# Kernel tuning notes

Measured on AMD Instinct MI355X. Metric: run time of the kernel, lower is better.

## Reference

```python
import jax, jax.numpy as jnp
import numpy as np

N = 100000      # nodes
E = 3200000     # edges (avg degree 32)
D = 128         # embed_dim
STEP = 1        # number of gnn_conv steps


def setup_inputs() -> dict:
    key = jax.random.key(0)
    k1, k2, k3, k4, k5 = jax.random.split(key, 5)
    hidden = jax.random.normal(k1, (N, D), dtype=jnp.float32)
    src = jax.random.randint(k2, (E,), 0, N)
    dst = jax.random.randint(k3, (E,), 0, N)
    # nn.Linear(D, 3D, bias=False) -> store transposed as [D, 3D] for h @ W
    W_h = jax.random.normal(k4, (D, 3 * D), dtype=jnp.float32) * 0.05
    W_hf = jax.random.normal(k5, (D, 2 * D), dtype=jnp.float32) * 0.05
    return {"hidden": hidden, "src": src, "dst": dst, "W_h": W_h, "W_hf": W_hf}


def _graph_conv(h, src, dst, n):
    # DGL GraphConv(norm='both', weight=False, bias=False):
    # h_dst = d_in(dst)^{-1/2} * sum_{(src->dst)} d_out(src)^{-1/2} * h_src
    ones = jnp.ones(src.shape[0], dtype=h.dtype)
    out_deg = jnp.clip(jax.ops.segment_sum(ones, src, num_segments=n), 1.0)
    in_deg = jnp.clip(jax.ops.segment_sum(ones, dst, num_segments=n), 1.0)
    h_norm = h * jax.lax.rsqrt(out_deg)[:, None]          # [N, D]
    agg = jax.ops.segment_sum(h_norm[src], dst, num_segments=n)  # [N, D]
    return agg * jax.lax.rsqrt(in_deg)[:, None]


def reference(hidden, src, dst, W_h, W_hf):
    n = hidden.shape[0]
    seqs = []
    for _ in range(STEP):
        h1, h2, h3 = jnp.split(hidden @ W_h, 3, axis=-1)   # each [N, D]
        conv = _graph_conv(h1, src, dst, n)                 # sparse aggregation
        f1, f2 = jnp.split(conv @ W_hf, 2, axis=-1)         # each [N, D]
        gate = jax.nn.relu(f1 + h2)
        hidden = h3 + gate * f2
        seqs.append(hidden)
    return hidden, jnp.stack(seqs, axis=1).mean(axis=1)
```

## Files before the change

kernel.cpp:

```cpp
#include <hip/hip_runtime.h>

#define N_NODES 100000
#define N_EDGES 3200000
#define DIM 128

#define NB 391
#define GCAP 9216
#define PCHUNK 4096

typedef __attribute__((ext_vector_type(8))) short bf16x8;
typedef __attribute__((ext_vector_type(4))) float f32x4;

__device__ __forceinline__ unsigned short f2bf(float x) {
    unsigned u = __float_as_uint(x);
    unsigned r = (u + 0x7FFF + ((u >> 16) & 1)) >> 16;
    return (unsigned short)r;
}

__device__ __forceinline__ bf16x8 load_bf8(const float* __restrict__ p) {
    float4 a0 = *reinterpret_cast<const float4*>(p);
    float4 a1 = *reinterpret_cast<const float4*>(p + 4);
    bf16x8 v;
    v[0] = (short)f2bf(a0.x); v[1] = (short)f2bf(a0.y);
    v[2] = (short)f2bf(a0.z); v[3] = (short)f2bf(a0.w);
    v[4] = (short)f2bf(a1.x); v[5] = (short)f2bf(a1.y);
    v[6] = (short)f2bf(a1.z); v[7] = (short)f2bf(a1.w);
    return v;
}

__device__ __forceinline__ void gld_lds16(const unsigned short* src, unsigned short* dst) {
    __builtin_amdgcn_global_load_lds(
        (const __attribute__((address_space(1))) unsigned int*)src,
        (__attribute__((address_space(3))) unsigned int*)dst, 16, 0, 0);
}

__global__ __launch_bounds__(256) void partition_kernel(const int* __restrict__ src,
                                                        const int* __restrict__ dst,
                                                        int* __restrict__ gcnt_d,
                                                        int* __restrict__ gcnt_s,
                                                        unsigned* __restrict__ bstore_d,
                                                        unsigned char* __restrict__ bstore_s) {
    __shared__ int hist_d[NB], cur_d[NB], hofs_d[NB];
    __shared__ int hist_s[NB], cur_s[NB], hofs_s[NB];
    __shared__ int vsc_d[512], vsc_s[512];
    __shared__ unsigned stage_d[PCHUNK];
    __shared__ unsigned short bmap_d[PCHUNK];
    __shared__ unsigned char stage_s[PCHUNK];
    __shared__ unsigned short bmap_s[PCHUNK];
    int t = threadIdx.x;
    for (int b = t; b < NB; b += 256) { hist_d[b] = 0; hist_s[b] = 0; }
    __syncthreads();
    int e0 = blockIdx.x * PCHUNK;
    int n = min(PCHUNK, N_EDGES - e0);
    for (int i = t; i < n; i += 256) {
        int s = src[e0 + i];
        int d = dst[e0 + i];
        atomicAdd(&hist_d[d >> 8], 1);
        atomicAdd(&hist_s[s >> 8], 1);
    }
    __syncthreads();
    for (int b = t; b < NB; b += 256) {
        hofs_d[b] = (hist_d[b] > 0) ? atomicAdd(&gcnt_d[b], hist_d[b]) : 0;
        hofs_s[b] = (hist_s[b] > 0) ? atomicAdd(&gcnt_s[b], hist_s[b]) : 0;
    }
    vsc_d[t]       = (t < NB) ? hist_d[t] : 0;
    vsc_d[t + 256] = (t + 256 < NB) ? hist_d[t + 256] : 0;
    vsc_s[t]       = (t < NB) ? hist_s[t] : 0;
    vsc_s[t + 256] = (t + 256 < NB) ? hist_s[t + 256] : 0;
    __syncthreads();
    for (int off = 1; off < 512; off <<= 1) {
        int d0 = (t >= off) ? vsc_d[t - off] : 0;
        int d1 = vsc_d[t + 256 - off];
        int s0 = (t >= off) ? vsc_s[t - off] : 0;
        int s1 = vsc_s[t + 256 - off];
        __syncthreads();
        vsc_d[t] += d0; vsc_d[t + 256] += d1;
        vsc_s[t] += s0; vsc_s[t + 256] += s1;
        __syncthreads();
    }
    for (int b = t; b < NB; b += 256) {
        cur_d[b] = b ? vsc_d[b - 1] : 0;
        cur_s[b] = b ? vsc_s[b - 1] : 0;
    }
    __syncthreads();
    for (int i = t; i < n; i += 256) {
        int s = src[e0 + i];
        int d = dst[e0 + i];
        int bd = d >> 8;
        int p = atomicAdd(&cur_d[bd], 1);
        stage_d[p] = ((unsigned)(d & 255) << 24) | (unsigned)s;
        bmap_d[p] = (unsigned short)bd;
        int bs = s >> 8;
        int ps = atomicAdd(&cur_s[bs], 1);
        stage_s[ps] = (unsigned char)(s & 255);
        bmap_s[ps] = (unsigned short)bs;
    }
    __syncthreads();
    for (int i = t; i < n; i += 256) {
        int bd = bmap_d[i];
        int excl = bd ? vsc_d[bd - 1] : 0;
        int gp = hofs_d[bd] + (i - excl);
        if (gp < GCAP) bstore_d[(size_t)bd * GCAP + gp] = stage_d[i];
        int bs2 = bmap_s[i];
        int excl2 = bs2 ? vsc_s[bs2 - 1] : 0;
        int gp2 = hofs_s[bs2] + (i - excl2);
        if (gp2 < GCAP) bstore_s[(size_t)bs2 * GCAP + gp2] = stage_s[i];
    }
}

__global__ void scanb_kernel(const int* __restrict__ gcnt_d, int* __restrict__ bucket_base,
                             int* __restrict__ row_start) {
    __shared__ int v[512];
    int t = threadIdx.x;
    v[t] = (t < NB) ? min(gcnt_d[t], GCAP) : 0;
    __syncthreads();
    for (int off = 1; off < 512; off <<= 1) {
        int x = (t >= off) ? v[t - off] : 0;
        __syncthreads();
        v[t] += x;
        __syncthreads();
    }
    if (t < NB) bucket_base[t + 1] = v[t];
    if (t == 0) {
        bucket_base[0] = 0;
        row_start[N_NODES] = v[NB - 1];
    }
}

__global__ __launch_bounds__(256) void count_kernel(const int* __restrict__ gcnt_s,
                                                    const unsigned char* __restrict__ bstore_s,
                                                    float* __restrict__ rn_out) {
    __shared__ int lcnt[256];
    int b = blockIdx.x;
    int t = threadIdx.x;
    lcnt[t] = 0;
    __syncthreads();
    int cnt = min(gcnt_s[b], GCAP);
    const unsigned char* bs = &bstore_s[(size_t)b * GCAP];
    for (int i = t; i < cnt; i += 256)
        atomicAdd(&lcnt[bs[i]], 1);
    __syncthreads();
    int node = b * 256 + t;
    if (node < N_NODES)
        rn_out[node] = rsqrtf((float)max(lcnt[t], 1));
}

__global__ __launch_bounds__(256) void fill2_kernel(const int* __restrict__ gcnt_d,
                                                    const unsigned* __restrict__ bstore_d,
                                                    const int* __restrict__ bucket_base,
                                                    int* __restrict__ col,
                                                    int* __restrict__ row_start,
                                                    float* __restrict__ rn_in) {
    __shared__ int lcnt[256];
    __shared__ int lpre[256];
    __shared__ int lcur[256];
    __shared__ int stage[GCAP];
    int b = blockIdx.x;
    int t = threadIdx.x;
    int node0 = b * 256;
    int nn = min(256, N_NODES - node0);
    lcnt[t] = 0;
    __syncthreads();
    int cnt = min(gcnt_d[b], GCAP);
    int base = bucket_base[b];
    const unsigned* bs = &bstore_d[(size_t)b * GCAP];
    for (int i = t; i < cnt; i += 256)
        atomicAdd(&lcnt[bs[i] >> 24], 1);
    __syncthreads();
    int myc = lcnt[t];
    lpre[t] = myc;
    __syncthreads();
    for (int off = 1; off < 256; off <<= 1) {
        int x = (t >= off) ? lpre[t - off] : 0;
        __syncthreads();
        lpre[t] += x;
        __syncthreads();
    }
    int excl = lpre[t] - myc;
    if (t < nn) {
        row_start[node0 + t] = base + excl;
        rn_in[node0 + t] = rsqrtf((float)max(myc, 1));
    }
    lcur[t] = excl;
    __syncthreads();
    for (int i = t; i < cnt; i += 256) {
        unsigned e = bs[i];
        int p = atomicAdd(&lcur[e >> 24], 1);
        stage[p] = (int)(e & 0xFFFFFF);
    }
    __syncthreads();
    for (int i = t; i < cnt; i += 256)
        col[base + i] = stage[i];
}

__global__ void packw_kernel(const float* __restrict__ W_h, const float* __restrict__ W_hf,
                             unsigned short* __restrict__ W1_t,
                             unsigned short* __restrict__ W23_t,
                             unsigned short* __restrict__ Wf_t) {
    int idx = blockIdx.x * 256 + threadIdx.x;
    if (idx < 16384) {
        int n = idx >> 7, k = idx & 127;
        W1_t[idx] = f2bf(W_h[k * 384 + n]);
    } else if (idx < 49152) {
        int j = idx - 16384;
        int n = j >> 7, k = j & 127;
        W23_t[j] = f2bf(W_h[k * 384 + 128 + n]);
    } else if (idx < 81920) {
        int j = idx - 49152;
        int n = j >> 7, k = j & 127;
        Wf_t[j] = f2bf(W_hf[k * 256 + n]);
    }
}

__global__ __launch_bounds__(256) void gemm1_mfma(const float* __restrict__ hidden,
                                                  const unsigned short* __restrict__ W1_t,
                                                  const float* __restrict__ rn_out,
                                                  unsigned short* __restrict__ h1n) {
    __shared__ __align__(16) unsigned short Bs[16384];
    int t = threadIdx.x;
    int row0 = blockIdx.x * 64;
    int lane = t & 63;
    int wave = t >> 6;
    int wr0 = wave * 16;
    int m = lane & 15;
    int q = lane >> 4;

    int arow = min(row0 + wr0 + m, N_NODES - 1);
    bf16x8 af[4];
#pragma unroll
    for (int kc = 0; kc < 4; ++kc)
        af[kc] = load_bf8(&hidden[(size_t)arow * 128 + kc * 32 + q * 8]);
    float s4[4];
#pragma unroll
    for (int reg = 0; reg < 4; ++reg) {
        int row = row0 + wr0 + q * 4 + reg;
        s4[reg] = (row < N_NODES) ? rn_out[row] : 0.f;
    }

#pragma unroll
    for (int i = 0; i < 8; ++i) {
        int G = i * 256 + t;
        int row = G >> 4;
        int kseg = G & 15;
        gld_lds16(&W1_t[row * 128 + ((kseg ^ (row & 7)) * 8)], &Bs[G * 8]);
    }
    __syncthreads();

    f32x4 accn[8];
#pragma unroll
    for (int nt = 0; nt < 8; ++nt) {
        f32x4 acc = {0.f, 0.f, 0.f, 0.f};
#pragma unroll
        for (int kc = 0; kc < 4; ++kc) {
            int g = (nt * 16 + m) * 16 + ((kc * 4 + q) ^ (m & 7));
            bf16x8 b = *reinterpret_cast<const bf16x8*>(&Bs[g * 8]);
            acc = __builtin_amdgcn_mfma_f32_16x16x32_bf16(af[kc], b, acc, 0, 0, 0);
        }
        accn[nt] = acc;
    }
    __syncthreads();

    unsigned short (*Sg)[136] = reinterpret_cast<unsigned short (*)[136]>(&Bs[0]);
#pragma unroll
    for (int nt = 0; nt < 8; ++nt)
#pragma unroll
        for (int reg = 0; reg < 4; ++reg)
            Sg[wr0 + q * 4 + reg][nt * 16 + m] = f2bf(accn[nt][reg] * s4[reg]);
    __syncthreads();
    int seg = (t & 15) * 8;
    int rb = t >> 4;
#pragma unroll
    for (int i = 0; i < 4; ++i) {
        int r = rb + i * 16;
        int row = row0 + r;
        if (row < N_NODES)
            *reinterpret_cast<int4*>(&h1n[row * 128 + seg]) =
                *reinterpret_cast<const int4*>(&Sg[r][seg]);
    }
}

__global__ __launch_bounds__(256) void aggregate_kernel(const unsigned* __restrict__ h1n,
                                                        const int* __restrict__ row_start,
                                                        const int* __restrict__ col,
                                                        const float* __restrict__ rn_in,
                                                        unsigned* __restrict__ conv_bf) {
    int wave = threadIdx.x >> 6;
    int lane = threadIdx.x & 63;
    int node = blockIdx.x * 4 + wave;
    if (node >= N_NODES) return;
    int start = row_start[node];
    int end = row_start[node + 1];
    float ax0 = 0.f, ax1 = 0.f, ay0 = 0.f, ay1 = 0.f;
    for (int j = start; j < end; j += 64) {
        int cnt = min(64, end - j);
        int myc = (lane < cnt) ? col[j + lane] : 0;
        int i = 0;
        for (; i + 32 <= cnt; i += 32) {
            unsigned u[16], v[16];
#pragma unroll
            for (int k = 0; k < 16; ++k) {
                int s = __builtin_amdgcn_readlane(myc, i + k);
                u[k] = h1n[s * 64 + lane];
            }
#pragma unroll
            for (int k = 0; k < 16; ++k) {
                int s = __builtin_amdgcn_readlane(myc, i + 16 + k);
                v[k] = h1n[s * 64 + lane];
            }
#pragma unroll
            for (int k = 0; k < 16; k += 2) {
                ax0 += __uint_as_float(u[k] << 16);
                ay0 += __uint_as_float(u[k] & 0xFFFF0000u);
                ax1 += __uint_as_float(u[k + 1] << 16);
                ay1 += __uint_as_float(u[k + 1] & 0xFFFF0000u);
            }
#pragma unroll
            for (int k = 0; k < 16; k += 2) {
                ax0 += __uint_as_float(v[k] << 16);
                ay0 += __uint_as_float(v[k] & 0xFFFF0000u);
                ax1 += __uint_as_float(v[k + 1] << 16);
                ay1 += __uint_as_float(v[k + 1] & 0xFFFF0000u);
            }
        }
        for (; i + 16 <= cnt; i += 16) {
            unsigned u[16];
#pragma unroll
            for (int k = 0; k < 16; ++k) {
                int s = __builtin_amdgcn_readlane(myc, i + k);
                u[k] = h1n[s * 64 + lane];
            }
#pragma unroll
            for (int k = 0; k < 16; k += 2) {
                ax0 += __uint_as_float(u[k] << 16);
                ay0 += __uint_as_float(u[k] & 0xFFFF0000u);
                ax1 += __uint_as_float(u[k + 1] << 16);
                ay1 += __uint_as_float(u[k + 1] & 0xFFFF0000u);
            }
        }
        for (; i + 4 <= cnt; i += 4) {
            unsigned u[4];
#pragma unroll
            for (int k = 0; k < 4; ++k) {
                int s = __builtin_amdgcn_readlane(myc, i + k);
                u[k] = h1n[s * 64 + lane];
            }
#pragma unroll
            for (int k = 0; k < 4; k += 2) {
                ax0 += __uint_as_float(u[k] << 16);
                ay0 += __uint_as_float(u[k] & 0xFFFF0000u);
                ax1 += __uint_as_float(u[k + 1] << 16);
                ay1 += __uint_as_float(u[k + 1] & 0xFFFF0000u);
            }
        }
        for (; i < cnt; ++i) {
            int s = __builtin_amdgcn_readlane(myc, i);
            unsigned u = h1n[s * 64 + lane];
            ax0 += __uint_as_float(u << 16);
            ay0 += __uint_as_float(u & 0xFFFF0000u);
        }
    }
    float rn = rn_in[node];
    float ax = ax0 + ax1, ay = ay0 + ay1;
    unsigned packed = ((unsigned)f2bf(ay * rn) << 16) | (unsigned)f2bf(ax * rn);
    conv_bf[node * 64 + lane] = packed;
}

__global__ __launch_bounds__(256) void final_mfma(const float* __restrict__ hidden,
                                                  const unsigned short* __restrict__ conv_bf,
                                                  const unsigned short* __restrict__ W23_t,
                                                  const unsigned short* __restrict__ Wf_t,
                                                  float* __restrict__ out) {
    __shared__ __align__(16) unsigned short Bst[2][8192];
    int t = threadIdx.x;
    int row0 = blockIdx.x * 64;
    int lane = t & 63;
    int wave = t >> 6;
    int wr0 = wave * 16;
    int m = lane & 15;
    int q = lane >> 4;

    int arow = min(row0 + wr0 + m, N_NODES - 1);
    bf16x8 ah[4], ac[4];
#pragma unroll
    for (int kc = 0; kc < 4; ++kc) {
        int o = arow * 128 + kc * 32 + q * 8;
        ah[kc] = load_bf8(&hidden[(size_t)o]);
        ac[kc] = *reinterpret_cast<const bf16x8*>(&conv_bf[o]);
    }

    auto stage = [&](int nt, int buf) {
#pragma unroll
        for (int i = 0; i < 4; ++i) {
            int rowin = t >> 4;
            int kseg = t & 15;
            int srow = ((i & 1) ? (nt + 8) : nt) * 16 + rowin;
            const unsigned short* Wp = (i < 2) ? W23_t : Wf_t;
            gld_lds16(&Wp[srow * 128 + ((kseg ^ (rowin & 7)) * 8)],
                      &Bst[buf][(i * 256 + t) * 8]);
        }
    };

    stage(0, 0);
    __syncthreads();

#pragma unroll
    for (int nt = 0; nt < 8; ++nt) {
        if (nt < 7) stage(nt + 1, (nt + 1) & 1);
        const unsigned short* Bb = Bst[nt & 1];
        f32x4 h2 = {0.f, 0.f, 0.f, 0.f}, h3 = {0.f, 0.f, 0.f, 0.f};
        f32x4 f1 = {0.f, 0.f, 0.f, 0.f}, f2 = {0.f, 0.f, 0.f, 0.f};
#pragma unroll
        for (int kc = 0; kc < 4; ++kc) {
            int ks = (kc * 4 + q) ^ (m & 7);
            bf16x8 b2  = *reinterpret_cast<const bf16x8*>(&Bb[(0 * 256 + m * 16 + ks) * 8]);
            bf16x8 b3  = *reinterpret_cast<const bf16x8*>(&Bb[(1 * 256 + m * 16 + ks) * 8]);
            bf16x8 bf1 = *reinterpret_cast<const bf16x8*>(&Bb[(2 * 256 + m * 16 + ks) * 8]);
            bf16x8 bf2 = *reinterpret_cast<const bf16x8*>(&Bb[(3 * 256 + m * 16 + ks) * 8]);
            h2 = __builtin_amdgcn_mfma_f32_16x16x32_bf16(ah[kc], b2, h2, 0, 0, 0);
            h3 = __builtin_amdgcn_mfma_f32_16x16x32_bf16(ah[kc], b3, h3, 0, 0, 0);
            f1 = __builtin_amdgcn_mfma_f32_16x16x32_bf16(ac[kc], bf1, f1, 0, 0, 0);
            f2 = __builtin_amdgcn_mfma_f32_16x16x32_bf16(ac[kc], bf2, f2, 0, 0, 0);
        }
        int colb = nt * 16 + m;
#pragma unroll
        for (int reg = 0; reg < 4; ++reg) {
            int row = row0 + wr0 + q * 4 + reg;
            float g = fmaxf(f1[reg] + h2[reg], 0.f);
            float o = h3[reg] + g * f2[reg];
            if (row < N_NODES) {
                out[(size_t)row * 128 + colb] = o;
                out[(size_t)(N_NODES + row) * 128 + colb] = o;
            }
        }
        __syncthreads();
    }
}

extern "C" void kernel_launch(void* const* d_in, const int* in_sizes, int n_in,
                              void* d_out, int out_size, void* d_ws, size_t ws_size,
                              hipStream_t stream) {
    const float* hidden = (const float*)d_in[0];
    const int* src = (const int*)d_in[1];
    const int* dst = (const int*)d_in[2];
    const float* W_h = (const float*)d_in[3];
    const float* W_hf = (const float*)d_in[4];
    float* out = (float*)d_out;

    auto align_up = [](size_t x) { return (x + 255) & ~(size_t)255; };
    char* p = (char*)d_ws;
    size_t off = 0;
    unsigned short* h1n = (unsigned short*)(p + off); off += align_up((size_t)N_NODES * 128 * 2);
    unsigned short* conv_bf = (unsigned short*)(p + off); off += align_up((size_t)N_NODES * 128 * 2);
    int* col = (int*)(p + off); off += align_up((size_t)N_EDGES * 4);
    unsigned* bstore_d = (unsigned*)(p + off); off += align_up((size_t)NB * GCAP * 4);
    unsigned char* bstore_s = (unsigned char*)(p + off); off += align_up((size_t)NB * GCAP);
    int* gcnt_d = (int*)(p + off); off += align_up((size_t)NB * 4);
    int* gcnt_s = (int*)(p + off); off += align_up((size_t)NB * 4);
    int* bucket_base = (int*)(p + off); off += align_up((size_t)(NB + 1) * 4);
    int* row_start = (int*)(p + off); off += align_up((size_t)(N_NODES + 1) * 4);
    float* rn_out = (float*)(p + off); off += align_up((size_t)N_NODES * 4);
    float* rn_in = (float*)(p + off); off += align_up((size_t)N_NODES * 4);
    unsigned short* W1_t = (unsigned short*)(p + off); off += align_up((size_t)128 * 128 * 2);
    unsigned short* W23_t = (unsigned short*)(p + off); off += align_up((size_t)256 * 128 * 2);
    unsigned short* Wf_t = (unsigned short*)(p + off); off += align_up((size_t)256 * 128 * 2);

    (void)hipMemsetAsync(gcnt_d, 0, (size_t)NB * 4, stream);
    (void)hipMemsetAsync(gcnt_s, 0, (size_t)NB * 4, stream);

    partition_kernel<<<(N_EDGES + PCHUNK - 1) / PCHUNK, 256, 0, stream>>>(
        src, dst, gcnt_d, gcnt_s, bstore_d, bstore_s);
    scanb_kernel<<<1, 512, 0, stream>>>(gcnt_d, bucket_base, row_start);
    count_kernel<<<NB, 256, 0, stream>>>(gcnt_s, bstore_s, rn_out);
    fill2_kernel<<<NB, 256, 0, stream>>>(gcnt_d, bstore_d, bucket_base, col, row_start, rn_in);
    packw_kernel<<<(81920 + 255) / 256, 256, 0, stream>>>(W_h, W_hf, W1_t, W23_t, Wf_t);
    gemm1_mfma<<<(N_NODES + 63) / 64, 256, 0, stream>>>(hidden, W1_t, rn_out, h1n);
    aggregate_kernel<<<(N_NODES + 3) / 4, 256, 0, stream>>>(
        (const unsigned*)h1n, row_start, col, rn_in, (unsigned*)conv_bf);
    final_mfma<<<(N_NODES + 63) / 64, 256, 0, stream>>>(hidden, conv_bf, W23_t, Wf_t, out);
}
```

Measured before the change: 412.5 us.

## Fuse neighbor aggregation into final MFMA kernel via LDS staging

Removes the separate aggregate kernel and conv_bf buffer. Each wave of the final kernel now gathers its 16 nodes' neighbor sums into shared memory, and those rows feed the MFMA A-operand directly, avoiding a global write and read of the bf16 conv tensor plus one launch. It also drops the 32-wide unrolled gather path, which reduces memory-level parallelism per wave. The aggregation now runs on only 1563 blocks with 16 sequential nodes per wave, so latency hiding for the gather may suffer.

```diff
diff --git a/kernel.cpp b/kernel.cpp
--- a/kernel.cpp
+++ b/kernel.cpp
@@ -279,33 +279,20 @@
     }
 }
 
-__global__ __launch_bounds__(256) void aggregate_kernel(const unsigned* __restrict__ h1n,
-                                                        const int* __restrict__ row_start,
-                                                        const int* __restrict__ col,
-                                                        const float* __restrict__ rn_in,
-                                                        unsigned* __restrict__ conv_bf) {
-    int wave = threadIdx.x >> 6;
-    int lane = threadIdx.x & 63;
-    int node = blockIdx.x * 4 + wave;
-    if (node >= N_NODES) return;
-    int start = row_start[node];
-    int end = row_start[node + 1];
+__device__ __forceinline__ unsigned gather_node(const unsigned* __restrict__ h1n,
+                                                const int* __restrict__ col,
+                                                int start, int end, int lane, float rn) {
     float ax0 = 0.f, ax1 = 0.f, ay0 = 0.f, ay1 = 0.f;
     for (int j = start; j < end; j += 64) {
         int cnt = min(64, end - j);
         int myc = (lane < cnt) ? col[j + lane] : 0;
         int i = 0;
-        for (; i + 32 <= cnt; i += 32) {
-            unsigned u[16], v[16];
+        for (; i + 16 <= cnt; i += 16) {
+            unsigned u[16];
 #pragma unroll
             for (int k = 0; k < 16; ++k) {
                 int s = __builtin_amdgcn_readlane(myc, i + k);
                 u[k] = h1n[s * 64 + lane];
-            }
-#pragma unroll
-            for (int k = 0; k < 16; ++k) {
-                int s = __builtin_amdgcn_readlane(myc, i + 16 + k);
-                v[k] = h1n[s * 64 + lane];
             }
 #pragma unroll
             for (int k = 0; k < 16; k += 2) {
@@ -314,28 +301,6 @@
                 ax1 += __uint_as_float(u[k + 1] << 16);
                 ay1 += __uint_as_float(u[k + 1] & 0xFFFF0000u);
             }
-#pragma unroll
-            for (int k = 0; k < 16; k += 2) {
-                ax0 += __uint_as_float(v[k] << 16);
-                ay0 += __uint_as_float(v[k] & 0xFFFF0000u);
-                ax1 += __uint_as_float(v[k + 1] << 16);
-                ay1 += __uint_as_float(v[k + 1] & 0xFFFF0000u);
-            }
-        }
-        for (; i + 16 <= cnt; i += 16) {
-            unsigned u[16];
-#pragma unroll
-            for (int k = 0; k < 16; ++k) {
-                int s = __builtin_amdgcn_readlane(myc, i + k);
-                u[k] = h1n[s * 64 + lane];
-            }
-#pragma unroll
-            for (int k = 0; k < 16; k += 2) {
-                ax0 += __uint_as_float(u[k] << 16);
-                ay0 += __uint_as_float(u[k] & 0xFFFF0000u);
-                ax1 += __uint_as_float(u[k + 1] << 16);
-                ay1 += __uint_as_float(u[k + 1] & 0xFFFF0000u);
-            }
         }
         for (; i + 4 <= cnt; i += 4) {
             unsigned u[4];
@@ -359,18 +324,19 @@
             ay0 += __uint_as_float(u & 0xFFFF0000u);
         }
     }
-    float rn = rn_in[node];
     float ax = ax0 + ax1, ay = ay0 + ay1;
-    unsigned packed = ((unsigned)f2bf(ay * rn) << 16) | (unsigned)f2bf(ax * rn);
-    conv_bf[node * 64 + lane] = packed;
-}
-
-__global__ __launch_bounds__(256) void final_mfma(const float* __restrict__ hidden,
-                                                  const unsigned short* __restrict__ conv_bf,
-                                                  const unsigned short* __restrict__ W23_t,
-                                                  const unsigned short* __restrict__ Wf_t,
-                                                  float* __restrict__ out) {
-    __shared__ __align__(16) unsigned short Bst[2][8192];
+    return ((unsigned)f2bf(ay * rn) << 16) | (unsigned)f2bf(ax * rn);
+}
+
+__global__ __launch_bounds__(256) void final_fused(const float* __restrict__ hidden,
+                                                   const unsigned* __restrict__ h1n,
+                                                   const int* __restrict__ row_start,
+                                                   const int* __restrict__ col,
+                                                   const float* __restrict__ rn_in,
+                                                   const unsigned short* __restrict__ W23_t,
+                                                   const unsigned short* __restrict__ Wf_t,
+                                                   float* __restrict__ out) {
+    __shared__ __align__(16) unsigned short LDSu[16384];
     int t = threadIdx.x;
     int row0 = blockIdx.x * 64;
     int lane = t & 63;
@@ -379,14 +345,27 @@
     int m = lane & 15;
     int q = lane >> 4;
 
+    unsigned short (*Sg)[136] = reinterpret_cast<unsigned short (*)[136]>(&LDSu[0]);
+    for (int ni = 0; ni < 16; ++ni) {
+        int node = row0 + wr0 + ni;
+        unsigned packed = 0;
+        if (node < N_NODES) {
+            int start = row_start[node];
+            int end = row_start[node + 1];
+            packed = gather_node(h1n, col, start, end, lane, rn_in[node]);
+        }
+        *reinterpret_cast<unsigned*>(&Sg[wr0 + ni][lane * 2]) = packed;
+    }
+    __syncthreads();
+
     int arow = min(row0 + wr0 + m, N_NODES - 1);
     bf16x8 ah[4], ac[4];
 #pragma unroll
     for (int kc = 0; kc < 4; ++kc) {
-        int o = arow * 128 + kc * 32 + q * 8;
-        ah[kc] = load_bf8(&hidden[(size_t)o]);
-        ac[kc] = *reinterpret_cast<const bf16x8*>(&conv_bf[o]);
-    }
+        ah[kc] = load_bf8(&hidden[(size_t)arow * 128 + kc * 32 + q * 8]);
+        ac[kc] = *reinterpret_cast<const bf16x8*>(&Sg[wr0 + m][kc * 32 + q * 8]);
+    }
+    __syncthreads();
 
     auto stage = [&](int nt, int buf) {
 #pragma unroll
@@ -396,7 +375,7 @@
             int srow = ((i & 1) ? (nt + 8) : nt) * 16 + rowin;
             const unsigned short* Wp = (i < 2) ? W23_t : Wf_t;
             gld_lds16(&Wp[srow * 128 + ((kseg ^ (rowin & 7)) * 8)],
-                      &Bst[buf][(i * 256 + t) * 8]);
+                      &LDSu[buf * 8192 + (i * 256 + t) * 8]);
         }
     };
 
@@ -406,7 +385,7 @@
 #pragma unroll
     for (int nt = 0; nt < 8; ++nt) {
         if (nt < 7) stage(nt + 1, (nt + 1) & 1);
-        const unsigned short* Bb = Bst[nt & 1];
+        const unsigned short* Bb = &LDSu[(nt & 1) * 8192];
         f32x4 h2 = {0.f, 0.f, 0.f, 0.f}, h3 = {0.f, 0.f, 0.f, 0.f};
         f32x4 f1 = {0.f, 0.f, 0.f, 0.f}, f2 = {0.f, 0.f, 0.f, 0.f};
 #pragma unroll
@@ -450,7 +429,6 @@
     char* p = (char*)d_ws;
     size_t off = 0;
     unsigned short* h1n = (unsigned short*)(p + off); off += align_up((size_t)N_NODES * 128 * 2);
-    unsigned short* conv_bf = (unsigned short*)(p + off); off += align_up((size_t)N_NODES * 128 * 2);
     int* col = (int*)(p + off); off += align_up((size_t)N_EDGES * 4);
     unsigned* bstore_d = (unsigned*)(p + off); off += align_up((size_t)NB * GCAP * 4);
     unsigned char* bstore_s = (unsigned char*)(p + off); off += align_up((size_t)NB * GCAP);
@@ -474,7 +452,6 @@
     fill2_kernel<<<NB, 256, 0, stream>>>(gcnt_d, bstore_d, bucket_base, col, row_start, rn_in);
     packw_kernel<<<(81920 + 255) / 256, 256, 0, stream>>>(W_h, W_hf, W1_t, W23_t, Wf_t);
     gemm1_mfma<<<(N_NODES + 63) / 64, 256, 0, stream>>>(hidden, W1_t, rn_out, h1n);
-    aggregate_kernel<<<(N_NODES + 3) / 4, 256, 0, stream>>>(
-        (const unsigned*)h1n, row_start, col, rn_in, (unsigned*)conv_bf);
-    final_mfma<<<(N_NODES + 63) / 64, 256, 0, stream>>>(hidden, conv_bf, W23_t, Wf_t, out);
-}
+    final_fused<<<(N_NODES + 63) / 64, 256, 0, stream>>>(
+        hidden, (const unsigned*)h1n, row_start, col, rn_in, W23_t, Wf_t, out);
+}
```

New measurement: 413.8 us. About the same (+0.3%).

## Sort CSR neighbors by source chunk and sweep chunks across 16 nodes per wave

Applied to the files above, without the earlier changes.

The CSR fill now groups each destination's neighbor list by source-index chunk (8192 nodes per chunk) and stores per-node, per-chunk counts as packed bytes. The aggregation kernel gives each wave 16 destination nodes and walks the source chunks in order, so that concurrent gathers touch a narrower range of h1n rows and hit L2 more often. The cost is 16 accumulator pairs per lane, more serialized small inner loops with less unrolling, per-node branching over chunk counts, and extra shared memory and atomics in the fill kernel. Per-chunk counts are held in 8 bits, which assumes no node has 256 or more in-edges from a single chunk.

```diff
diff --git a/kernel.cpp b/kernel.cpp
--- a/kernel.cpp
+++ b/kernel.cpp
@@ -7,6 +7,7 @@
 #define NB 391
 #define GCAP 9216
 #define PCHUNK 4096
+#define NCHUNK 13
 
 typedef __attribute__((ext_vector_type(8))) short bf16x8;
 typedef __attribute__((ext_vector_type(4))) float f32x4;
@@ -150,25 +151,34 @@
                                                     const int* __restrict__ bucket_base,
                                                     int* __restrict__ col,
                                                     int* __restrict__ row_start,
-                                                    float* __restrict__ rn_in) {
-    __shared__ int lcnt[256];
+                                                    float* __restrict__ rn_in,
+                                                    unsigned char* __restrict__ cntb) {
+    __shared__ int cnt[256 * NCHUNK];
     __shared__ int lpre[256];
-    __shared__ int lcur[256];
     __shared__ int stage[GCAP];
     int b = blockIdx.x;
     int t = threadIdx.x;
     int node0 = b * 256;
     int nn = min(256, N_NODES - node0);
-    lcnt[t] = 0;
-    __syncthreads();
-    int cnt = min(gcnt_d[b], GCAP);
+    for (int i = t; i < 256 * NCHUNK; i += 256) cnt[i] = 0;
+    __syncthreads();
+    int ccnt = min(gcnt_d[b], GCAP);
     int base = bucket_base[b];
     const unsigned* bs = &bstore_d[(size_t)b * GCAP];
-    for (int i = t; i < cnt; i += 256)
-        atomicAdd(&lcnt[bs[i] >> 24], 1);
-    __syncthreads();
-    int myc = lcnt[t];
-    lpre[t] = myc;
+    for (int i = t; i < ccnt; i += 256) {
+        unsigned e = bs[i];
+        int idx = (int)(e >> 24) * NCHUNK + (int)((e & 0xFFFFFF) >> 13);
+        atomicAdd(&cnt[idx], 1);
+    }
+    __syncthreads();
+    int ccs[NCHUNK];
+#pragma unroll
+    for (int c = 0; c < NCHUNK; ++c) ccs[c] = cnt[t * NCHUNK + c];
+    int deg = 0;
+    int myofs[NCHUNK];
+#pragma unroll
+    for (int c = 0; c < NCHUNK; ++c) { myofs[c] = deg; deg += ccs[c]; }
+    lpre[t] = deg;
     __syncthreads();
     for (int off = 1; off < 256; off <<= 1) {
         int x = (t >= off) ? lpre[t - off] : 0;
@@ -176,20 +186,31 @@
         lpre[t] += x;
         __syncthreads();
     }
-    int excl = lpre[t] - myc;
+    int nodeExcl = lpre[t] - deg;
+#pragma unroll
+    for (int c = 0; c < NCHUNK; ++c) cnt[t * NCHUNK + c] = nodeExcl + myofs[c];
     if (t < nn) {
-        row_start[node0 + t] = base + excl;
-        rn_in[node0 + t] = rsqrtf((float)max(myc, 1));
-    }
-    lcur[t] = excl;
-    __syncthreads();
-    for (int i = t; i < cnt; i += 256) {
+        row_start[node0 + t] = base + nodeExcl;
+        rn_in[node0 + t] = rsqrtf((float)max(deg, 1));
+        unsigned w0 = (unsigned)ccs[0] | ((unsigned)ccs[1] << 8) |
+                      ((unsigned)ccs[2] << 16) | ((unsigned)ccs[3] << 24);
+        unsigned w1 = (unsigned)ccs[4] | ((unsigned)ccs[5] << 8) |
+                      ((unsigned)ccs[6] << 16) | ((unsigned)ccs[7] << 24);
+        unsigned w2 = (unsigned)ccs[8] | ((unsigned)ccs[9] << 8) |
+                      ((unsigned)ccs[10] << 16) | ((unsigned)ccs[11] << 24);
+        unsigned w3 = (unsigned)ccs[12];
+        int4 v = make_int4((int)w0, (int)w1, (int)w2, (int)w3);
+        *reinterpret_cast<int4*>(&cntb[(size_t)(node0 + t) * 16]) = v;
+    }
+    __syncthreads();
+    for (int i = t; i < ccnt; i += 256) {
         unsigned e = bs[i];
-        int p = atomicAdd(&lcur[e >> 24], 1);
+        int idx = (int)(e >> 24) * NCHUNK + (int)((e & 0xFFFFFF) >> 13);
+        int p = atomicAdd(&cnt[idx], 1);
         stage[p] = (int)(e & 0xFFFFFF);
     }
     __syncthreads();
-    for (int i = t; i < cnt; i += 256)
+    for (int i = t; i < ccnt; i += 256)
         col[base + i] = stage[i];
 }
 
@@ -283,86 +304,68 @@
                                                         const int* __restrict__ row_start,
                                                         const int* __restrict__ col,
                                                         const float* __restrict__ rn_in,
+                                                        const unsigned char* __restrict__ cntb,
                                                         unsigned* __restrict__ conv_bf) {
     int wave = threadIdx.x >> 6;
     int lane = threadIdx.x & 63;
-    int node = blockIdx.x * 4 + wave;
-    if (node >= N_NODES) return;
-    int start = row_start[node];
-    int end = row_start[node + 1];
-    float ax0 = 0.f, ax1 = 0.f, ay0 = 0.f, ay1 = 0.f;
-    for (int j = start; j < end; j += 64) {
-        int cnt = min(64, end - j);
-        int myc = (lane < cnt) ? col[j + lane] : 0;
-        int i = 0;
-        for (; i + 32 <= cnt; i += 32) {
-            unsigned u[16], v[16];
-#pragma unroll
-            for (int k = 0; k < 16; ++k) {
-                int s = __builtin_amdgcn_readlane(myc, i + k);
-                u[k] = h1n[s * 64 + lane];
+    int nbase = blockIdx.x * 64 + wave * 16;
+    if (nbase >= N_NODES) return;
+    int nmax = min(16, N_NODES - nbase);
+    int ofs = 0;
+    int4 cv = make_int4(0, 0, 0, 0);
+    if (lane < nmax) {
+        ofs = row_start[nbase + lane];
+        cv = *reinterpret_cast<const int4*>(&cntb[(size_t)(nbase + lane) * 16]);
+    }
+    float ax[16], ay[16];
+#pragma unroll
+    for (int i = 0; i < 16; ++i) { ax[i] = 0.f; ay[i] = 0.f; }
+
+    for (int c = 0; c < NCHUNK; ++c) {
+        int cw = (c < 4) ? cv.x : (c < 8) ? cv.y : (c < 12) ? cv.z : cv.w;
+        int cntv = (cw >> ((c & 3) * 8)) & 255;
+#pragma unroll
+        for (int i = 0; i < 16; ++i) {
+            int s_cnt = __builtin_amdgcn_readlane(cntv, i);
+            if (s_cnt == 0) continue;
+            int s_start = __builtin_amdgcn_readlane(ofs, i);
+            for (int j = 0; j < s_cnt; j += 64) {
+                int c2 = min(64, s_cnt - j);
+                int myc = (lane < c2) ? col[s_start + j + lane] : 0;
+                int k = 0;
+                for (; k + 4 <= c2; k += 4) {
+                    unsigned u[4];
+#pragma unroll
+                    for (int kk = 0; kk < 4; ++kk) {
+                        int s = __builtin_amdgcn_readlane(myc, k + kk);
+                        u[kk] = h1n[s * 64 + lane];
+                    }
+#pragma unroll
+                    for (int kk = 0; kk < 4; ++kk) {
+                        ax[i] += __uint_as_float(u[kk] << 16);
+                        ay[i] += __uint_as_float(u[kk] & 0xFFFF0000u);
+                    }
+                }
+                for (; k < c2; ++k) {
+                    int s = __builtin_amdgcn_readlane(myc, k);
+                    unsigned u = h1n[s * 64 + lane];
+                    ax[i] += __uint_as_float(u << 16);
+                    ay[i] += __uint_as_float(u & 0xFFFF0000u);
+                }
             }
-#pragma unroll
-            for (int k = 0; k < 16; ++k) {
-                int s = __builtin_amdgcn_readlane(myc, i + 16 + k);
-                v[k] = h1n[s * 64 + lane];
-            }
-#pragma unroll
-            for (int k = 0; k < 16; k += 2) {
-                ax0 += __uint_as_float(u[k] << 16);
-                ay0 += __uint_as_float(u[k] & 0xFFFF0000u);
-                ax1 += __uint_as_float(u[k + 1] << 16);
-                ay1 += __uint_as_float(u[k + 1] & 0xFFFF0000u);
-            }
-#pragma unroll
-            for (int k = 0; k < 16; k += 2) {
-                ax0 += __uint_as_float(v[k] << 16);
-                ay0 += __uint_as_float(v[k] & 0xFFFF0000u);
-                ax1 += __uint_as_float(v[k + 1] << 16);
-                ay1 += __uint_as_float(v[k + 1] & 0xFFFF0000u);
-            }
-        }
-        for (; i + 16 <= cnt; i += 16) {
-            unsigned u[16];
-#pragma unroll
-            for (int k = 0; k < 16; ++k) {
-                int s = __builtin_amdgcn_readlane(myc, i + k);
-                u[k] = h1n[s * 64 + lane];
-            }
-#pragma unroll
-            for (int k = 0; k < 16; k += 2) {
-                ax0 += __uint_as_float(u[k] << 16);
-                ay0 += __uint_as_float(u[k] & 0xFFFF0000u);
-                ax1 += __uint_as_float(u[k + 1] << 16);
-                ay1 += __uint_as_float(u[k + 1] & 0xFFFF0000u);
-            }
-        }
-        for (; i + 4 <= cnt; i += 4) {
-            unsigned u[4];
-#pragma unroll
-            for (int k = 0; k < 4; ++k) {
-                int s = __builtin_amdgcn_readlane(myc, i + k);
-                u[k] = h1n[s * 64 + lane];
-            }
-#pragma unroll
-            for (int k = 0; k < 4; k += 2) {
-                ax0 += __uint_as_float(u[k] << 16);
-                ay0 += __uint_as_float(u[k] & 0xFFFF0000u);
-                ax1 += __uint_as_float(u[k + 1] << 16);
-                ay1 += __uint_as_float(u[k + 1] & 0xFFFF0000u);
-            }
-        }
-        for (; i < cnt; ++i) {
-            int s = __builtin_amdgcn_readlane(myc, i);
-            unsigned u = h1n[s * 64 + lane];
-            ax0 += __uint_as_float(u << 16);
-            ay0 += __uint_as_float(u & 0xFFFF0000u);
-        }
-    }
-    float rn = rn_in[node];
-    float ax = ax0 + ax1, ay = ay0 + ay1;
-    unsigned packed = ((unsigned)f2bf(ay * rn) << 16) | (unsigned)f2bf(ax * rn);
-    conv_bf[node * 64 + lane] = packed;
+        }
+        ofs += cntv;
+    }
+#pragma unroll
+    for (int i = 0; i < 16; ++i) {
+        if (i < nmax) {
+            int node = nbase + i;
+            float rni = rn_in[node];
+            unsigned packed = ((unsigned)f2bf(ay[i] * rni) << 16) |
+                              (unsigned)f2bf(ax[i] * rni);
+            conv_bf[node * 64 + lane] = packed;
+        }
+    }
 }
 
 __global__ __launch_bounds__(256) void final_mfma(const float* __restrict__ hidden,
@@ -454,6 +457,7 @@
     int* col = (int*)(p + off); off += align_up((size_t)N_EDGES * 4);
     unsigned* bstore_d = (unsigned*)(p + off); off += align_up((size_t)NB * GCAP * 4);
     unsigned char* bstore_s = (unsigned char*)(p + off); off += align_up((size_t)NB * GCAP);
+    unsigned char* cntb = (unsigned char*)(p + off); off += align_up((size_t)N_NODES * 16);
     int* gcnt_d = (int*)(p + off); off += align_up((size_t)NB * 4);
     int* gcnt_s = (int*)(p + off); off += align_up((size_t)NB * 4);
     int* bucket_base = (int*)(p + off); off += align_up((size_t)(NB + 1) * 4);
@@ -471,10 +475,11 @@
         src, dst, gcnt_d, gcnt_s, bstore_d, bstore_s);
     scanb_kernel<<<1, 512, 0, stream>>>(gcnt_d, bucket_base, row_start);
     count_kernel<<<NB, 256, 0, stream>>>(gcnt_s, bstore_s, rn_out);
-    fill2_kernel<<<NB, 256, 0, stream>>>(gcnt_d, bstore_d, bucket_base, col, row_start, rn_in);
+    fill2_kernel<<<NB, 256, 0, stream>>>(gcnt_d, bstore_d, bucket_base, col, row_start,
+                                         rn_in, cntb);
     packw_kernel<<<(81920 + 255) / 256, 256, 0, stream>>>(W_h, W_hf, W1_t, W23_t, Wf_t);
     gemm1_mfma<<<(N_NODES + 63) / 64, 256, 0, stream>>>(hidden, W1_t, rn_out, h1n);
-    aggregate_kernel<<<(N_NODES + 3) / 4, 256, 0, stream>>>(
-        (const unsigned*)h1n, row_start, col, rn_in, (unsigned*)conv_bf);
+    aggregate_kernel<<<(N_NODES + 63) / 64, 256, 0, stream>>>(
+        (const unsigned*)h1n, row_start, col, rn_in, cntb, (unsigned*)conv_bf);
     final_mfma<<<(N_NODES + 63) / 64, 256, 0, stream>>>(hidden, conv_bf, W23_t, Wf_t, out);
 }
```

Result: slower. 510.4 us (+23.7%).

## Sort CSR neighbor lists by source chunk and drop 32-wide gather unroll

Applied to the files above, without the earlier changes.

The CSR fill kernel now counts edges per (destination node, source-id chunk of 8192) instead of per node. Each node's neighbors are therefore placed grouped by coarse source range, so the gathers in aggregation touch nearby rows and may get better cache locality. The aggregation kernel also loses its 32-edge unrolled path and relies on the 16-edge path, which lowers register pressure but exposes fewer loads in flight. The fill kernel pays for a larger shared-memory count array and per-thread chunk offsets.

```diff
diff --git a/kernel.cpp b/kernel.cpp
--- a/kernel.cpp
+++ b/kernel.cpp
@@ -7,6 +7,7 @@
 #define NB 391
 #define GCAP 9216
 #define PCHUNK 4096
+#define NCHUNK 13
 
 typedef __attribute__((ext_vector_type(8))) short bf16x8;
 typedef __attribute__((ext_vector_type(4))) float f32x4;
@@ -151,24 +152,32 @@
                                                     int* __restrict__ col,
                                                     int* __restrict__ row_start,
                                                     float* __restrict__ rn_in) {
-    __shared__ int lcnt[256];
+    __shared__ int cnt[256 * NCHUNK];
     __shared__ int lpre[256];
-    __shared__ int lcur[256];
     __shared__ int stage[GCAP];
     int b = blockIdx.x;
     int t = threadIdx.x;
     int node0 = b * 256;
     int nn = min(256, N_NODES - node0);
-    lcnt[t] = 0;
-    __syncthreads();
-    int cnt = min(gcnt_d[b], GCAP);
+    for (int i = t; i < 256 * NCHUNK; i += 256) cnt[i] = 0;
+    __syncthreads();
+    int ccnt = min(gcnt_d[b], GCAP);
     int base = bucket_base[b];
     const unsigned* bs = &bstore_d[(size_t)b * GCAP];
-    for (int i = t; i < cnt; i += 256)
-        atomicAdd(&lcnt[bs[i] >> 24], 1);
-    __syncthreads();
-    int myc = lcnt[t];
-    lpre[t] = myc;
+    for (int i = t; i < ccnt; i += 256) {
+        unsigned e = bs[i];
+        int idx = (int)(e >> 24) * NCHUNK + (int)((e & 0xFFFFFF) >> 13);
+        atomicAdd(&cnt[idx], 1);
+    }
+    __syncthreads();
+    int ccs[NCHUNK];
+#pragma unroll
+    for (int c = 0; c < NCHUNK; ++c) ccs[c] = cnt[t * NCHUNK + c];
+    int deg = 0;
+    int myofs[NCHUNK];
+#pragma unroll
+    for (int c = 0; c < NCHUNK; ++c) { myofs[c] = deg; deg += ccs[c]; }
+    lpre[t] = deg;
     __syncthreads();
     for (int off = 1; off < 256; off <<= 1) {
         int x = (t >= off) ? lpre[t - off] : 0;
@@ -176,20 +185,22 @@
         lpre[t] += x;
         __syncthreads();
     }
-    int excl = lpre[t] - myc;
+    int nodeExcl = lpre[t] - deg;
+#pragma unroll
+    for (int c = 0; c < NCHUNK; ++c) cnt[t * NCHUNK + c] = nodeExcl + myofs[c];
     if (t < nn) {
-        row_start[node0 + t] = base + excl;
-        rn_in[node0 + t] = rsqrtf((float)max(myc, 1));
-    }
-    lcur[t] = excl;
-    __syncthreads();
-    for (int i = t; i < cnt; i += 256) {
+        row_start[node0 + t] = base + nodeExcl;
+        rn_in[node0 + t] = rsqrtf((float)max(deg, 1));
+    }
+    __syncthreads();
+    for (int i = t; i < ccnt; i += 256) {
         unsigned e = bs[i];
-        int p = atomicAdd(&lcur[e >> 24], 1);
+        int idx = (int)(e >> 24) * NCHUNK + (int)((e & 0xFFFFFF) >> 13);
+        int p = atomicAdd(&cnt[idx], 1);
         stage[p] = (int)(e & 0xFFFFFF);
     }
     __syncthreads();
-    for (int i = t; i < cnt; i += 256)
+    for (int i = t; i < ccnt; i += 256)
         col[base + i] = stage[i];
 }
 
@@ -295,33 +306,6 @@
         int cnt = min(64, end - j);
         int myc = (lane < cnt) ? col[j + lane] : 0;
         int i = 0;
-        for (; i + 32 <= cnt; i += 32) {
-            unsigned u[16], v[16];
-#pragma unroll
-            for (int k = 0; k < 16; ++k) {
-                int s = __builtin_amdgcn_readlane(myc, i + k);
-                u[k] = h1n[s * 64 + lane];
-            }
-#pragma unroll
-            for (int k = 0; k < 16; ++k) {
-                int s = __builtin_amdgcn_readlane(myc, i + 16 + k);
-                v[k] = h1n[s * 64 + lane];
-            }
-#pragma unroll
-            for (int k = 0; k < 16; k += 2) {
-                ax0 += __uint_as_float(u[k] << 16);
-                ay0 += __uint_as_float(u[k] & 0xFFFF0000u);
-                ax1 += __uint_as_float(u[k + 1] << 16);
-                ay1 += __uint_as_float(u[k + 1] & 0xFFFF0000u);
-            }
-#pragma unroll
-            for (int k = 0; k < 16; k += 2) {
-                ax0 += __uint_as_float(v[k] << 16);
-                ay0 += __uint_as_float(v[k] & 0xFFFF0000u);
-                ax1 += __uint_as_float(v[k + 1] << 16);
-                ay1 += __uint_as_float(v[k + 1] & 0xFFFF0000u);
-            }
-        }
         for (; i + 16 <= cnt; i += 16) {
             unsigned u[16];
 #pragma unroll
```

Measured after the change: 413.8 us. No clear change (+0.3%).
